# Performance work log

Hardware: AMD Instinct MI355X
Metric: run time of the kernel (lower is better)

The kernel has to match this reference:

```python
import jax, jax.numpy as jnp
import numpy as np
from jax import lax

B, P, E, H, V, S = 128, 196, 2048, 512, 10000, 21


def setup_inputs() -> dict:
    key = jax.random.key(0)
    ks = jax.random.split(key, 16)
    r = lambda k, shape, s=0.02: (jax.random.normal(k, shape, jnp.float32) * s)
    return {
        "img_features": jax.random.normal(ks[0], (B, P, E), jnp.float32),
        "captions": jax.random.randint(ks[1], (B, S), 0, V),
        "U_w": r(ks[2], (H, H)), "U_b": jnp.zeros((H,), jnp.float32),
        "W_w": r(ks[3], (E, H)), "W_b": jnp.zeros((H,), jnp.float32),
        "v_w": r(ks[4], (H, 1)), "v_b": jnp.zeros((1,), jnp.float32),
        "init_h_w": r(ks[5], (E, H)), "init_h_b": jnp.zeros((H,), jnp.float32),
        "init_c_w": r(ks[6], (E, H)), "init_c_b": jnp.zeros((H,), jnp.float32),
        "f_beta_w": r(ks[7], (H, E)), "f_beta_b": jnp.zeros((E,), jnp.float32),
        "out_w": r(ks[8], (H, V)), "out_b": jnp.zeros((V,), jnp.float32),
        "emb": r(ks[9], (V, H)),
        "lstm_Wih": r(ks[10], (H + E, 4 * H)), "lstm_Whh": r(ks[11], (H, 4 * H)),
        "lstm_bih": jnp.zeros((4 * H,), jnp.float32), "lstm_bhh": jnp.zeros((4 * H,), jnp.float32),
    }


def reference(img_features, captions, U_w, U_b, W_w, W_b, v_w, v_b,
              init_h_w, init_h_b, init_c_w, init_c_b, f_beta_w, f_beta_b,
              out_w, out_b, emb, lstm_Wih, lstm_Whh, lstm_bih, lstm_bhh):
    batch = img_features.shape[0]
    T = captions.shape[1] - 1  # max_timespan (static)

    # init LSTM state from mean-pooled image features
    avg = img_features.mean(axis=1)                       # [B, E]
    h0 = jnp.tanh(avg @ init_h_w + init_h_b)              # [B, H]
    c0 = jnp.tanh(avg @ init_c_w + init_c_b)              # [B, H]

    # precompute W(img_features) once; it does not depend on h
    W_s = img_features @ W_w + W_b                        # [B, P, H]

    # in training mode the original feeds the embedding of word 0 every step
    emb0 = jnp.broadcast_to(emb[0], (batch, emb.shape[1]))  # [B, H]

    def step(carry, _):
        h, c = carry
        # additive attention
        att = jnp.tanh(W_s + (h @ U_w + U_b)[:, None, :])      # [B, P, H]
        e = (att @ v_w)[..., 0] + v_b[0]                        # [B, P]
        alpha = jax.nn.softmax(e, axis=1)                       # [B, P]
        context = jnp.einsum('bp,bpe->be', alpha, img_features) # [B, E]
        # gated context
        gate = jax.nn.sigmoid(h @ f_beta_w + f_beta_b)          # [B, E]
        x = jnp.concatenate([emb0, gate * context], axis=1)     # [B, H+E]
        # LSTMCell (torch gate order i, f, g, o)
        gates = x @ lstm_Wih + lstm_bih + h @ lstm_Whh + lstm_bhh  # [B, 4H]
        i, f, g, o = jnp.split(gates, 4, axis=1)
        i = jax.nn.sigmoid(i); f = jax.nn.sigmoid(f)
        g = jnp.tanh(g); o = jax.nn.sigmoid(o)
        c_new = f * c + i * g
        h_new = o * jnp.tanh(c_new)
        out = h_new @ out_w + out_b                             # [B, V] (dropout = identity, eval)
        return (h_new, c_new), (out, alpha)

    (_, _), (preds, alphas) = lax.scan(step, (h0, c0), None, length=T)
    preds = jnp.transpose(preds, (1, 0, 2))    # [B, T, V]
    alphas = jnp.transpose(alphas, (1, 0, 2))  # [B, T, P]
    return preds, alphas
```

## Files before the change

### kernel.cpp

```cpp
#include <hip/hip_runtime.h>
#include <stdint.h>


typedef unsigned short u16;
typedef unsigned int u32;
typedef __attribute__((ext_vector_type(8))) short bf16x8;
typedef __attribute__((ext_vector_type(4))) float f32x4;

__device__ __forceinline__ float bf2f(u16 u) { return __uint_as_float(((u32)u) << 16); }
__device__ __forceinline__ u16 f2bf(float f) {
  u32 x = __float_as_uint(f);
  u32 r = x + 0x7fffu + ((x >> 16) & 1u);
  return (u16)(r >> 16);
}
__device__ __forceinline__ float tanh_f(float x) {
  x = fminf(15.f, fmaxf(-15.f, x));
  float e = __expf(2.f * x);
  return 1.f - 2.f * __builtin_amdgcn_rcpf(e + 1.f);
}
__device__ __forceinline__ float sigm_f(float x) {
  x = fminf(30.f, fmaxf(-30.f, x));
  return __builtin_amdgcn_rcpf(1.f + __expf(-x));
}

__global__ __launch_bounds__(256) void k_f32_to_bf16(const float* __restrict__ in,
                                                     u16* __restrict__ out) {
  size_t i = ((size_t)blockIdx.x * 256 + threadIdx.x) * 8;
  float4 v0 = *(const float4*)(in + i);
  float4 v1 = *(const float4*)(in + i + 4);
  union { u16 u[8]; uint4 v; } r;
  r.u[0] = f2bf(v0.x); r.u[1] = f2bf(v0.y); r.u[2] = f2bf(v0.z); r.u[3] = f2bf(v0.w);
  r.u[4] = f2bf(v1.x); r.u[5] = f2bf(v1.y); r.u[6] = f2bf(v1.z); r.u[7] = f2bf(v1.w);
  *(uint4*)(out + i) = r.v;
}

__global__ __launch_bounds__(256) void k_avg(const u16* __restrict__ imgb,
                                             u16* __restrict__ avgb) {
  int b = blockIdx.y;
  int c0 = blockIdx.x * 512 + threadIdx.x * 2;
  const u32* p0 = (const u32*)(imgb + (size_t)b * 196 * 2048 + c0);
  float s0 = 0.f, s1 = 0.f;
  for (int p = 0; p < 196; ++p) {
    u32 v = p0[(size_t)p * 1024];
    s0 += bf2f((u16)(v & 0xffff));
    s1 += bf2f((u16)(v >> 16));
  }
  const float inv = 1.f / 196.f;
  u32 o = ((u32)f2bf(s1 * inv) << 16) | (u32)f2bf(s0 * inv);
  *(u32*)(avgb + (size_t)b * 2048 + c0) = o;
}

__global__ __launch_bounds__(256) void k_transpose_bf16(const float* __restrict__ in,
                                                        int R, int C, int Cpad,
                                                        u16* __restrict__ out, int out_ld) {
  __shared__ float tile[32][33];
  int c0 = blockIdx.x * 32, r0 = blockIdx.y * 32;
  int tx = threadIdx.x, ty = threadIdx.y;
#pragma unroll
  for (int i = 0; i < 32; i += 8) {
    int r = r0 + ty + i, c = c0 + tx;
    tile[ty + i][tx] = (r < R && c < C) ? in[(size_t)r * C + c] : 0.f;
  }
  __syncthreads();
#pragma unroll
  for (int i = 0; i < 32; i += 8) {
    int c = c0 + ty + i, r = r0 + tx;
    if (c < Cpad && r < R) out[(size_t)c * out_ld + r] = f2bf(tile[tx][ty + i]);
  }
}

__global__ __launch_bounds__(256) void k_cbias(const float* __restrict__ emb,
                                               const float* __restrict__ Wih,
                                               const float* __restrict__ bih,
                                               const float* __restrict__ bhh,
                                               float* __restrict__ cb) {
  __shared__ float e0[512];
  int tid = threadIdx.x;
  for (int i = tid; i < 512; i += 256) e0[i] = emb[i];
  __syncthreads();
  int n = blockIdx.x * 256 + tid;
  float s = bih[n] + bhh[n];
  for (int k = 0; k < 512; ++k) s += e0[k] * Wih[(size_t)k * 2048 + n];
  cb[n] = s;
}

enum { EPI_WS = 0, EPI_TANH_H, EPI_TANH_C, EPI_F32, EPI_GATE, EPI_OUT };

template <int EPI>
__global__ __launch_bounds__(256) void k_gemm64(
    const u16* __restrict__ A, const u16* __restrict__ BT, int K, int Ntiles,
    const float* __restrict__ bias, float* __restrict__ outF, u16* __restrict__ outB,
    u16* __restrict__ outB2, const float* __restrict__ ctx, long out_ld, int ncap) {
  __shared__ __align__(16) u16 Asm[64 * 72];
  __shared__ __align__(16) u16 Bsm[64 * 72];
  int bid = blockIdx.x;
  int mt = bid / Ntiles, nt = bid % Ntiles;
  long m0 = (long)mt * 64, n0 = (long)nt * 64;
  int tid = threadIdx.x, lane = tid & 63, w = tid >> 6;
  int srow = tid >> 3, schk = tid & 7;
  f32x4 acc[4] = {};
  const u16* Ap0 = A + (m0 + srow) * K + schk * 8;
  const u16* Ap1 = A + (m0 + srow + 32) * K + schk * 8;
  const u16* Bp0 = BT + (n0 + srow) * K + schk * 8;
  const u16* Bp1 = BT + (n0 + srow + 32) * K + schk * 8;
  u16* Aw0 = Asm + srow * 72 + schk * 8;
  u16* Aw1 = Asm + (srow + 32) * 72 + schk * 8;
  u16* Bw0 = Bsm + srow * 72 + schk * 8;
  u16* Bw1 = Bsm + (srow + 32) * 72 + schk * 8;
  const u16* Ar = Asm + (w * 16 + (lane & 15)) * 72 + (lane >> 4) * 8;
  const u16* Br = Bsm + (lane & 15) * 72 + (lane >> 4) * 8;
  for (int k0 = 0; k0 < K; k0 += 64) {
    uint4 a0 = *(const uint4*)(Ap0 + k0);
    uint4 a1 = *(const uint4*)(Ap1 + k0);
    uint4 b0 = *(const uint4*)(Bp0 + k0);
    uint4 b1 = *(const uint4*)(Bp1 + k0);
    __syncthreads();
    *(uint4*)Aw0 = a0;
    *(uint4*)Aw1 = a1;
    *(uint4*)Bw0 = b0;
    *(uint4*)Bw1 = b1;
    __syncthreads();
#pragma unroll
    for (int kk = 0; kk < 2; ++kk) {
      bf16x8 af = *(const bf16x8*)(Ar + kk * 32);
#pragma unroll
      for (int sn = 0; sn < 4; ++sn) {
        bf16x8 bfr = *(const bf16x8*)(Br + sn * 16 * 72 + kk * 32);
        acc[sn] = __builtin_amdgcn_mfma_f32_16x16x32_bf16(af, bfr, acc[sn], 0, 0, 0);
      }
    }
  }
  int cb = lane & 15, rb = (lane >> 4) * 4;
#pragma unroll
  for (int sn = 0; sn < 4; ++sn) {
#pragma unroll
    for (int r = 0; r < 4; ++r) {
      long m = m0 + w * 16 + rb + r;
      long n = n0 + sn * 16 + cb;
      float v = acc[sn][r];
      if (EPI == EPI_WS) {
        outB[m * 512 + n] = f2bf(v + bias[n]);
      } else if (EPI == EPI_TANH_H) {
        u16 hv = f2bf(tanh_f(v + bias[n]));
        outB[m * 512 + n] = hv;
        outB2[m * 2560 + n] = hv;
      } else if (EPI == EPI_TANH_C) {
        outF[m * 512 + n] = tanh_f(v + bias[n]);
      } else if (EPI == EPI_F32) {
        outF[m * out_ld + n] = v + bias[n];
      } else if (EPI == EPI_GATE) {
        float g = sigm_f(v + bias[n]);
        outB[m * 2560 + n] = f2bf(g * ctx[m * 2048 + n]);
      } else {
        if (n < ncap) outF[m * out_ld + n] = v + bias[n];
      }
    }
  }
}

__global__ __launch_bounds__(512) void k_attn_e(const u16* __restrict__ Ws,
                                                const float* __restrict__ hU,
                                                const float* __restrict__ v_w,
                                                float* __restrict__ alpha_buf,
                                                float* __restrict__ alphas_out) {
  int b = blockIdx.x, tid = threadIdx.x, lane = tid & 63, w = tid >> 6;
  __shared__ float hU_s[512], v_s[512], e_s[200];
  hU_s[tid] = hU[b * 512 + tid];
  v_s[tid] = v_w[tid];
  __syncthreads();
  for (int p = w; p < 196; p += 8) {
    uint4 pk = *(const uint4*)(Ws + ((size_t)b * 196 + p) * 512 + lane * 8);
    const u16* u = (const u16*)&pk;
    float s = 0.f;
#pragma unroll
    for (int j = 0; j < 8; ++j) {
      int h = lane * 8 + j;
      s += tanh_f(bf2f(u[j]) + hU_s[h]) * v_s[h];
    }
#pragma unroll
    for (int off = 32; off; off >>= 1) s += __shfl_xor(s, off);
    if (lane == 0) e_s[p] = s;
  }
  __syncthreads();
  if (w == 0) {
    float mx = -1e30f;
    for (int q = lane; q < 196; q += 64) mx = fmaxf(mx, e_s[q]);
#pragma unroll
    for (int off = 32; off; off >>= 1) mx = fmaxf(mx, __shfl_xor(mx, off));
    float ssum = 0.f;
    for (int q = lane; q < 196; q += 64) {
      float ex = __expf(e_s[q] - mx);
      e_s[q] = ex;
      ssum += ex;
    }
#pragma unroll
    for (int off = 32; off; off >>= 1) ssum += __shfl_xor(ssum, off);
    float inv = 1.f / ssum;
    for (int q = lane; q < 196; q += 64) e_s[q] *= inv;
  }
  __syncthreads();
  if (tid < 196) {
    float a = e_s[tid];
    alpha_buf[b * 196 + tid] = a;
    alphas_out[(size_t)b * 3920 + tid] = a;
  }
}

__global__ __launch_bounds__(512) void k_context(const float* __restrict__ alpha_buf,
                                                 const u16* __restrict__ imgb,
                                                 float* __restrict__ ctx) {
  int b = blockIdx.x >> 1, half = blockIdx.x & 1, tid = threadIdx.x;
  __shared__ float al[196];
  if (tid < 196) al[tid] = alpha_buf[b * 196 + tid];
  __syncthreads();
  int c0 = half * 1024 + tid * 2;
  const u32* base = (const u32*)(imgb + (size_t)b * 196 * 2048 + c0);
  float a0 = 0.f, a1 = 0.f;
#pragma unroll 4
  for (int p = 0; p < 196; ++p) {
    u32 v = base[(size_t)p * 1024];
    float ap = al[p];
    a0 += ap * bf2f((u16)(v & 0xffff));
    a1 += ap * bf2f((u16)(v >> 16));
  }
  ctx[(size_t)b * 2048 + c0] = a0;
  ctx[(size_t)b * 2048 + c0 + 1] = a1;
}

__global__ __launch_bounds__(256) void k_lstm_cell(const float* __restrict__ gates,
                                                   float* __restrict__ c,
                                                   u16* __restrict__ hb,
                                                   u16* __restrict__ Abuf) {
  int idx = blockIdx.x * 256 + threadIdx.x;
  int b = idx >> 9, n = idx & 511;
  const float* g = gates + (size_t)b * 2048;
  float i = sigm_f(g[n]);
  float f = sigm_f(g[512 + n]);
  float gg = tanh_f(g[1024 + n]);
  float o = sigm_f(g[1536 + n]);
  float cn = f * c[idx] + i * gg;
  float h = o * tanh_f(cn);
  c[idx] = cn;
  u16 hv = f2bf(h);
  hb[idx] = hv;
  Abuf[(size_t)b * 2560 + 2048 + n] = hv;
}

extern "C" void kernel_launch(void* const* d_in, const int* in_sizes, int n_in,
                              void* d_out, int out_size, void* d_ws, size_t ws_size,
                              hipStream_t stream) {
  const float* img = (const float*)d_in[0];
  const float* U_w = (const float*)d_in[2];
  const float* U_b = (const float*)d_in[3];
  const float* W_w = (const float*)d_in[4];
  const float* W_b = (const float*)d_in[5];
  const float* v_w = (const float*)d_in[6];
  const float* ih_w = (const float*)d_in[8];
  const float* ih_b = (const float*)d_in[9];
  const float* ic_w = (const float*)d_in[10];
  const float* ic_b = (const float*)d_in[11];
  const float* fb_w = (const float*)d_in[12];
  const float* fb_b = (const float*)d_in[13];
  const float* out_w = (const float*)d_in[14];
  const float* out_b = (const float*)d_in[15];
  const float* emb = (const float*)d_in[16];
  const float* Wih = (const float*)d_in[17];
  const float* Whh = (const float*)d_in[18];
  const float* bih = (const float*)d_in[19];
  const float* bhh = (const float*)d_in[20];
  float* preds = (float*)d_out;
  float* alphas = (float*)d_out + 25600000;

  char* ws = (char*)d_ws;
  size_t off = 0;
  auto alloc = [&](size_t bytes) {
    void* p = ws + off;
    off = (off + bytes + 255) & ~(size_t)255;
    return p;
  };
  u16* imgb = (u16*)alloc((size_t)128 * 196 * 2048 * 2);
  u16* avgb = (u16*)alloc((size_t)128 * 2048 * 2);
  u16* WsB = (u16*)alloc((size_t)128 * 196 * 512 * 2);
  u16* WwT = (u16*)alloc((size_t)512 * 2048 * 2);
  u16* UwT = (u16*)alloc((size_t)512 * 512 * 2);
  u16* ihT = (u16*)alloc((size_t)512 * 2048 * 2);
  u16* icT = (u16*)alloc((size_t)512 * 2048 * 2);
  u16* fbT = (u16*)alloc((size_t)2048 * 512 * 2);
  u16* WcT = (u16*)alloc((size_t)2048 * 2560 * 2);
  u16* owT = (u16*)alloc((size_t)10048 * 512 * 2);
  float* cbias = (float*)alloc(2048 * 4);
  u16* hb = (u16*)alloc((size_t)128 * 512 * 2);
  float* cbuf = (float*)alloc((size_t)128 * 512 * 4);
  float* hU = (float*)alloc((size_t)128 * 512 * 4);
  float* albuf = (float*)alloc((size_t)128 * 196 * 4);
  float* ctx = (float*)alloc((size_t)128 * 2048 * 4);
  u16* Abuf = (u16*)alloc((size_t)128 * 2560 * 2);
  float* gates = (float*)alloc((size_t)128 * 2048 * 4);
  if (off > ws_size) return;
  (void)in_sizes; (void)n_in; (void)out_size;

  dim3 tb(32, 8);
  k_f32_to_bf16<<<25088, 256, 0, stream>>>(img, imgb);
  k_avg<<<dim3(4, 128), 256, 0, stream>>>(imgb, avgb);
  k_transpose_bf16<<<dim3(16, 64), tb, 0, stream>>>(W_w, 2048, 512, 512, WwT, 2048);
  k_transpose_bf16<<<dim3(16, 16), tb, 0, stream>>>(U_w, 512, 512, 512, UwT, 512);
  k_transpose_bf16<<<dim3(16, 64), tb, 0, stream>>>(ih_w, 2048, 512, 512, ihT, 2048);
  k_transpose_bf16<<<dim3(16, 64), tb, 0, stream>>>(ic_w, 2048, 512, 512, icT, 2048);
  k_transpose_bf16<<<dim3(64, 16), tb, 0, stream>>>(fb_w, 512, 2048, 2048, fbT, 512);
  k_transpose_bf16<<<dim3(314, 16), tb, 0, stream>>>(out_w, 512, 10000, 10048, owT, 512);
  k_transpose_bf16<<<dim3(64, 64), tb, 0, stream>>>(Wih + 512 * 2048, 2048, 2048, 2048, WcT, 2560);
  k_transpose_bf16<<<dim3(64, 16), tb, 0, stream>>>(Whh, 512, 2048, 2048, WcT + 2048, 2560);
  k_cbias<<<8, 256, 0, stream>>>(emb, Wih, bih, bhh, cbias);
  k_gemm64<EPI_WS><<<392 * 8, 256, 0, stream>>>(imgb, WwT, 2048, 8, W_b, nullptr, WsB,
                                                nullptr, nullptr, 0L, 0);
  k_gemm64<EPI_TANH_H><<<16, 256, 0, stream>>>(avgb, ihT, 2048, 8, ih_b, nullptr, hb,
                                               Abuf + 2048, nullptr, 0L, 0);
  k_gemm64<EPI_TANH_C><<<16, 256, 0, stream>>>(avgb, icT, 2048, 8, ic_b, cbuf, nullptr,
                                               nullptr, nullptr, 0L, 0);

  for (int t = 0; t < 20; ++t) {
    k_gemm64<EPI_F32><<<16, 256, 0, stream>>>(hb, UwT, 512, 8, U_b, hU, nullptr,
                                              nullptr, nullptr, 512L, 0);
    k_attn_e<<<128, 512, 0, stream>>>(WsB, hU, v_w, albuf, alphas + (size_t)t * 196);
    k_context<<<256, 512, 0, stream>>>(albuf, imgb, ctx);
    k_gemm64<EPI_GATE><<<64, 256, 0, stream>>>(hb, fbT, 512, 32, fb_b, nullptr, Abuf,
                                               nullptr, ctx, 0L, 0);
    k_gemm64<EPI_F32><<<64, 256, 0, stream>>>(Abuf, WcT, 2560, 32, cbias, gates,
                                              nullptr, nullptr, nullptr, 2048L, 0);
    k_lstm_cell<<<256, 256, 0, stream>>>(gates, cbuf, hb, Abuf);
    k_gemm64<EPI_OUT><<<2 * 157, 256, 0, stream>>>(hb, owT, 512, 157, out_b,
                                                   preds + (size_t)t * 10000, nullptr,
                                                   nullptr, nullptr, 200000L, 10000);
  }
}
```

Baseline: 2.584 ms.

## Fuse attention and context, fold LSTM cell into gate GEMM, batch output projection

Merges the h·U projection, attention scores, softmax and context reduction into one per-batch kernel. The LSTM cell moves into the gate GEMM epilogue, which relies on permuting the combined weight columns and bias so each tile holds interleaved i/f/g/o. All hidden states are saved so the vocabulary projection runs once after the loop as a single 128x128-tile GEMM, and the W_s GEMM also uses that larger tile. Double-buffered A inputs avoid a race between steps. This cuts per-step launches from seven to three and replaces twenty small output GEMMs with one large one, at the cost of a serial 512x512 matvec inside each attention block.

```diff
diff --git a/kernel.cpp b/kernel.cpp
--- a/kernel.cpp
+++ b/kernel.cpp
@@ -50,6 +50,7 @@
   *(u32*)(avgb + (size_t)b * 2048 + c0) = o;
 }
 
+template <bool PERM>
 __global__ __launch_bounds__(256) void k_transpose_bf16(const float* __restrict__ in,
                                                         int R, int C, int Cpad,
                                                         u16* __restrict__ out, int out_ld) {
@@ -65,7 +66,10 @@
 #pragma unroll
   for (int i = 0; i < 32; i += 8) {
     int c = c0 + ty + i, r = r0 + tx;
-    if (c < Cpad && r < R) out[(size_t)c * out_ld + r] = f2bf(tile[tx][ty + i]);
+    if (c < Cpad && r < R) {
+      int co = PERM ? ((c & 511) * 4 + (c >> 9)) : c;
+      out[(size_t)co * out_ld + r] = f2bf(tile[tx][ty + i]);
+    }
   }
 }
 
@@ -81,16 +85,17 @@
   int n = blockIdx.x * 256 + tid;
   float s = bih[n] + bhh[n];
   for (int k = 0; k < 512; ++k) s += e0[k] * Wih[(size_t)k * 2048 + n];
-  cb[n] = s;
-}
-
-enum { EPI_WS = 0, EPI_TANH_H, EPI_TANH_C, EPI_F32, EPI_GATE, EPI_OUT };
+  cb[(n & 511) * 4 + (n >> 9)] = s;
+}
+
+enum { EPI_TANH_H = 0, EPI_TANH_C, EPI_GATE, EPI_LSTM };
 
 template <int EPI>
 __global__ __launch_bounds__(256) void k_gemm64(
     const u16* __restrict__ A, const u16* __restrict__ BT, int K, int Ntiles,
-    const float* __restrict__ bias, float* __restrict__ outF, u16* __restrict__ outB,
-    u16* __restrict__ outB2, const float* __restrict__ ctx, long out_ld, int ncap) {
+    const float* __restrict__ bias, float* __restrict__ outF,
+    u16* __restrict__ outB, u16* __restrict__ outB2, u16* __restrict__ outB3,
+    const float* __restrict__ ctx, int tstep) {
   __shared__ __align__(16) u16 Asm[64 * 72];
   __shared__ __align__(16) u16 Bsm[64 * 72];
   int bid = blockIdx.x;
@@ -131,119 +136,202 @@
     }
   }
   int cb = lane & 15, rb = (lane >> 4) * 4;
-#pragma unroll
-  for (int sn = 0; sn < 4; ++sn) {
-#pragma unroll
-    for (int r = 0; r < 4; ++r) {
-      long m = m0 + w * 16 + rb + r;
-      long n = n0 + sn * 16 + cb;
-      float v = acc[sn][r];
-      if (EPI == EPI_WS) {
-        outB[m * 512 + n] = f2bf(v + bias[n]);
-      } else if (EPI == EPI_TANH_H) {
-        u16 hv = f2bf(tanh_f(v + bias[n]));
-        outB[m * 512 + n] = hv;
-        outB2[m * 2560 + n] = hv;
-      } else if (EPI == EPI_TANH_C) {
-        outF[m * 512 + n] = tanh_f(v + bias[n]);
-      } else if (EPI == EPI_F32) {
-        outF[m * out_ld + n] = v + bias[n];
-      } else if (EPI == EPI_GATE) {
-        float g = sigm_f(v + bias[n]);
-        outB[m * 2560 + n] = f2bf(g * ctx[m * 2048 + n]);
-      } else {
-        if (n < ncap) outF[m * out_ld + n] = v + bias[n];
+  if constexpr (EPI == EPI_LSTM) {
+    __shared__ float gtile[64][68];
+#pragma unroll
+    for (int sn = 0; sn < 4; ++sn)
+#pragma unroll
+      for (int r = 0; r < 4; ++r)
+        gtile[w * 16 + rb + r][sn * 16 + cb] = acc[sn][r] + bias[n0 + sn * 16 + cb];
+    __syncthreads();
+#pragma unroll
+    for (int i = 0; i < 4; ++i) {
+      int idx = tid * 4 + i;
+      int m = idx >> 4, chl = idx & 15;
+      float iv = gtile[m][chl * 4 + 0];
+      float fv = gtile[m][chl * 4 + 1];
+      float gv = gtile[m][chl * 4 + 2];
+      float ov = gtile[m][chl * 4 + 3];
+      long bg = m0 + m;
+      int ch = (int)(n0 >> 2) + chl;
+      long ci = bg * 512 + ch;
+      float cn = sigm_f(fv) * outF[ci] + sigm_f(iv) * tanh_f(gv);
+      float h = sigm_f(ov) * tanh_f(cn);
+      outF[ci] = cn;
+      u16 hv = f2bf(h);
+      outB[ci] = hv;
+      outB2[bg * 2560 + 2048 + ch] = hv;
+      outB3[((long)tstep * 128 + bg) * 512 + ch] = hv;
+    }
+  } else {
+#pragma unroll
+    for (int sn = 0; sn < 4; ++sn) {
+#pragma unroll
+      for (int r = 0; r < 4; ++r) {
+        long m = m0 + w * 16 + rb + r;
+        long n = n0 + sn * 16 + cb;
+        float v = acc[sn][r];
+        if (EPI == EPI_TANH_H) {
+          u16 hv = f2bf(tanh_f(v + bias[n]));
+          outB[m * 512 + n] = hv;
+          outB2[m * 2560 + 2048 + n] = hv;
+        } else if (EPI == EPI_TANH_C) {
+          outF[m * 512 + n] = tanh_f(v + bias[n]);
+        } else {
+          outB[m * 2560 + n] = f2bf(sigm_f(v + bias[n]) * ctx[m * 2048 + n]);
+        }
       }
     }
   }
 }
 
-__global__ __launch_bounds__(512) void k_attn_e(const u16* __restrict__ Ws,
-                                                const float* __restrict__ hU,
-                                                const float* __restrict__ v_w,
-                                                float* __restrict__ alpha_buf,
-                                                float* __restrict__ alphas_out) {
+enum { EPI128_WS = 0, EPI128_OUT };
+
+template <int EPI>
+__global__ __launch_bounds__(256) void k_gemm128(
+    const u16* __restrict__ A, const u16* __restrict__ BT, int K, int Ntiles,
+    const float* __restrict__ bias, float* __restrict__ outF,
+    u16* __restrict__ outB, int ncap) {
+  __shared__ __align__(16) u16 Asm[128 * 72];
+  __shared__ __align__(16) u16 Bsm[128 * 72];
+  int bid = blockIdx.x;
+  int mt = bid / Ntiles, nt = bid % Ntiles;
+  long m0 = (long)mt * 128, n0 = (long)nt * 128;
+  int tid = threadIdx.x, lane = tid & 63, w = tid >> 6;
+  int wr = w >> 1, wc = w & 1;
+  int srow = tid >> 3, schk = tid & 7;
+  f32x4 acc[4][4] = {};
+  const u16* Ap = A + (m0 + srow) * K + schk * 8;
+  const u16* Bp = BT + (n0 + srow) * K + schk * 8;
+  u16* Aw = Asm + srow * 72 + schk * 8;
+  u16* Bw = Bsm + srow * 72 + schk * 8;
+  const u16* Ar = Asm + (wr * 64 + (lane & 15)) * 72 + (lane >> 4) * 8;
+  const u16* Br = Bsm + (wc * 64 + (lane & 15)) * 72 + (lane >> 4) * 8;
+  for (int k0 = 0; k0 < K; k0 += 64) {
+    uint4 a0 = *(const uint4*)(Ap + k0);
+    uint4 a1 = *(const uint4*)(Ap + (size_t)32 * K + k0);
+    uint4 a2 = *(const uint4*)(Ap + (size_t)64 * K + k0);
+    uint4 a3 = *(const uint4*)(Ap + (size_t)96 * K + k0);
+    uint4 b0 = *(const uint4*)(Bp + k0);
+    uint4 b1 = *(const uint4*)(Bp + (size_t)32 * K + k0);
+    uint4 b2 = *(const uint4*)(Bp + (size_t)64 * K + k0);
+    uint4 b3 = *(const uint4*)(Bp + (size_t)96 * K + k0);
+    __syncthreads();
+    *(uint4*)Aw = a0;
+    *(uint4*)(Aw + 32 * 72) = a1;
+    *(uint4*)(Aw + 64 * 72) = a2;
+    *(uint4*)(Aw + 96 * 72) = a3;
+    *(uint4*)Bw = b0;
+    *(uint4*)(Bw + 32 * 72) = b1;
+    *(uint4*)(Bw + 64 * 72) = b2;
+    *(uint4*)(Bw + 96 * 72) = b3;
+    __syncthreads();
+#pragma unroll
+    for (int kk = 0; kk < 2; ++kk) {
+      bf16x8 af[4], bfv[4];
+#pragma unroll
+      for (int i = 0; i < 4; ++i) {
+        af[i] = *(const bf16x8*)(Ar + i * 16 * 72 + kk * 32);
+        bfv[i] = *(const bf16x8*)(Br + i * 16 * 72 + kk * 32);
+      }
+#pragma unroll
+      for (int sm = 0; sm < 4; ++sm)
+#pragma unroll
+        for (int sn = 0; sn < 4; ++sn)
+          acc[sm][sn] = __builtin_amdgcn_mfma_f32_16x16x32_bf16(af[sm], bfv[sn],
+                                                                acc[sm][sn], 0, 0, 0);
+    }
+  }
+  int cb = lane & 15, rb = (lane >> 4) * 4;
+#pragma unroll
+  for (int sm = 0; sm < 4; ++sm) {
+#pragma unroll
+    for (int sn = 0; sn < 4; ++sn) {
+#pragma unroll
+      for (int r = 0; r < 4; ++r) {
+        long m = m0 + wr * 64 + sm * 16 + rb + r;
+        long n = n0 + wc * 64 + sn * 16 + cb;
+        float v = acc[sm][sn][r];
+        if (EPI == EPI128_WS) {
+          outB[m * 512 + n] = f2bf(v + bias[n]);
+        } else {
+          if (n < ncap) {
+            long t = m >> 7, b = m & 127;
+            outF[b * 200000 + t * 10000 + n] = v + bias[n];
+          }
+        }
+      }
+    }
+  }
+}
+
+__global__ __launch_bounds__(512) void k_attn_ctx(
+    const u16* __restrict__ hb, const u16* __restrict__ UwB,
+    const float* __restrict__ U_b, const float* __restrict__ v_w,
+    const u16* __restrict__ WsB, const u16* __restrict__ imgb,
+    float* __restrict__ ctx, float* __restrict__ alphas_t) {
   int b = blockIdx.x, tid = threadIdx.x, lane = tid & 63, w = tid >> 6;
-  __shared__ float hU_s[512], v_s[512], e_s[200];
-  hU_s[tid] = hU[b * 512 + tid];
+  __shared__ float h_s[512], hu_s[512], v_s[512], al_s[200];
+  h_s[tid] = bf2f(hb[b * 512 + tid]);
   v_s[tid] = v_w[tid];
   __syncthreads();
+  {
+    float s = U_b[tid];
+    const u16* up = UwB + tid;
+#pragma unroll 8
+    for (int k = 0; k < 512; ++k) s += h_s[k] * bf2f(up[(size_t)k * 512]);
+    hu_s[tid] = s;
+  }
+  __syncthreads();
   for (int p = w; p < 196; p += 8) {
-    uint4 pk = *(const uint4*)(Ws + ((size_t)b * 196 + p) * 512 + lane * 8);
+    uint4 pk = *(const uint4*)(WsB + ((size_t)b * 196 + p) * 512 + lane * 8);
     const u16* u = (const u16*)&pk;
-    float s = 0.f;
+    float e = 0.f;
 #pragma unroll
     for (int j = 0; j < 8; ++j) {
-      int h = lane * 8 + j;
-      s += tanh_f(bf2f(u[j]) + hU_s[h]) * v_s[h];
-    }
-#pragma unroll
-    for (int off = 32; off; off >>= 1) s += __shfl_xor(s, off);
-    if (lane == 0) e_s[p] = s;
+      int hch = lane * 8 + j;
+      e += tanh_f(bf2f(u[j]) + hu_s[hch]) * v_s[hch];
+    }
+#pragma unroll
+    for (int off = 32; off; off >>= 1) e += __shfl_xor(e, off);
+    if (lane == 0) al_s[p] = e;
   }
   __syncthreads();
   if (w == 0) {
     float mx = -1e30f;
-    for (int q = lane; q < 196; q += 64) mx = fmaxf(mx, e_s[q]);
+    for (int q = lane; q < 196; q += 64) mx = fmaxf(mx, al_s[q]);
 #pragma unroll
     for (int off = 32; off; off >>= 1) mx = fmaxf(mx, __shfl_xor(mx, off));
     float ssum = 0.f;
     for (int q = lane; q < 196; q += 64) {
-      float ex = __expf(e_s[q] - mx);
-      e_s[q] = ex;
+      float ex = __expf(al_s[q] - mx);
+      al_s[q] = ex;
       ssum += ex;
     }
 #pragma unroll
     for (int off = 32; off; off >>= 1) ssum += __shfl_xor(ssum, off);
     float inv = 1.f / ssum;
-    for (int q = lane; q < 196; q += 64) e_s[q] *= inv;
-  }
-  __syncthreads();
-  if (tid < 196) {
-    float a = e_s[tid];
-    alpha_buf[b * 196 + tid] = a;
-    alphas_out[(size_t)b * 3920 + tid] = a;
-  }
-}
-
-__global__ __launch_bounds__(512) void k_context(const float* __restrict__ alpha_buf,
-                                                 const u16* __restrict__ imgb,
-                                                 float* __restrict__ ctx) {
-  int b = blockIdx.x >> 1, half = blockIdx.x & 1, tid = threadIdx.x;
-  __shared__ float al[196];
-  if (tid < 196) al[tid] = alpha_buf[b * 196 + tid];
-  __syncthreads();
-  int c0 = half * 1024 + tid * 2;
-  const u32* base = (const u32*)(imgb + (size_t)b * 196 * 2048 + c0);
-  float a0 = 0.f, a1 = 0.f;
-#pragma unroll 4
+    for (int q = lane; q < 196; q += 64) al_s[q] *= inv;
+  }
+  __syncthreads();
+  if (tid < 196) alphas_t[(size_t)b * 3920 + tid] = al_s[tid];
+  const u32* ib = (const u32*)(imgb + (size_t)b * 196 * 2048) + tid;
+  float a0 = 0.f, a1 = 0.f, a2 = 0.f, a3 = 0.f;
+#pragma unroll 2
   for (int p = 0; p < 196; ++p) {
-    u32 v = base[(size_t)p * 1024];
-    float ap = al[p];
-    a0 += ap * bf2f((u16)(v & 0xffff));
-    a1 += ap * bf2f((u16)(v >> 16));
-  }
-  ctx[(size_t)b * 2048 + c0] = a0;
-  ctx[(size_t)b * 2048 + c0 + 1] = a1;
-}
-
-__global__ __launch_bounds__(256) void k_lstm_cell(const float* __restrict__ gates,
-                                                   float* __restrict__ c,
-                                                   u16* __restrict__ hb,
-                                                   u16* __restrict__ Abuf) {
-  int idx = blockIdx.x * 256 + threadIdx.x;
-  int b = idx >> 9, n = idx & 511;
-  const float* g = gates + (size_t)b * 2048;
-  float i = sigm_f(g[n]);
-  float f = sigm_f(g[512 + n]);
-  float gg = tanh_f(g[1024 + n]);
-  float o = sigm_f(g[1536 + n]);
-  float cn = f * c[idx] + i * gg;
-  float h = o * tanh_f(cn);
-  c[idx] = cn;
-  u16 hv = f2bf(h);
-  hb[idx] = hv;
-  Abuf[(size_t)b * 2560 + 2048 + n] = hv;
+    float ap = al_s[p];
+    u32 v0 = ib[(size_t)p * 1024];
+    u32 v1 = ib[(size_t)p * 1024 + 512];
+    a0 += ap * bf2f((u16)(v0 & 0xffff));
+    a1 += ap * bf2f((u16)(v0 >> 16));
+    a2 += ap * bf2f((u16)(v1 & 0xffff));
+    a3 += ap * bf2f((u16)(v1 >> 16));
+  }
+  float* cp = ctx + (size_t)b * 2048;
+  cp[tid * 2] = a0;
+  cp[tid * 2 + 1] = a1;
+  cp[1024 + tid * 2] = a2;
+  cp[1024 + tid * 2 + 1] = a3;
 }
 
 extern "C" void kernel_launch(void* const* d_in, const int* in_sizes, int n_in,
@@ -282,54 +370,50 @@
   u16* avgb = (u16*)alloc((size_t)128 * 2048 * 2);
   u16* WsB = (u16*)alloc((size_t)128 * 196 * 512 * 2);
   u16* WwT = (u16*)alloc((size_t)512 * 2048 * 2);
-  u16* UwT = (u16*)alloc((size_t)512 * 512 * 2);
+  u16* UwB = (u16*)alloc((size_t)512 * 512 * 2);
   u16* ihT = (u16*)alloc((size_t)512 * 2048 * 2);
   u16* icT = (u16*)alloc((size_t)512 * 2048 * 2);
   u16* fbT = (u16*)alloc((size_t)2048 * 512 * 2);
   u16* WcT = (u16*)alloc((size_t)2048 * 2560 * 2);
-  u16* owT = (u16*)alloc((size_t)10048 * 512 * 2);
+  u16* owT = (u16*)alloc((size_t)10112 * 512 * 2);
   float* cbias = (float*)alloc(2048 * 4);
   u16* hb = (u16*)alloc((size_t)128 * 512 * 2);
   float* cbuf = (float*)alloc((size_t)128 * 512 * 4);
-  float* hU = (float*)alloc((size_t)128 * 512 * 4);
-  float* albuf = (float*)alloc((size_t)128 * 196 * 4);
   float* ctx = (float*)alloc((size_t)128 * 2048 * 4);
-  u16* Abuf = (u16*)alloc((size_t)128 * 2560 * 2);
-  float* gates = (float*)alloc((size_t)128 * 2048 * 4);
+  u16* AbufA = (u16*)alloc((size_t)128 * 2560 * 2);
+  u16* AbufB = (u16*)alloc((size_t)128 * 2560 * 2);
+  u16* hAll = (u16*)alloc((size_t)2560 * 512 * 2);
   if (off > ws_size) return;
   (void)in_sizes; (void)n_in; (void)out_size;
 
   dim3 tb(32, 8);
   k_f32_to_bf16<<<25088, 256, 0, stream>>>(img, imgb);
+  k_f32_to_bf16<<<128, 256, 0, stream>>>(U_w, UwB);
   k_avg<<<dim3(4, 128), 256, 0, stream>>>(imgb, avgb);
-  k_transpose_bf16<<<dim3(16, 64), tb, 0, stream>>>(W_w, 2048, 512, 512, WwT, 2048);
-  k_transpose_bf16<<<dim3(16, 16), tb, 0, stream>>>(U_w, 512, 512, 512, UwT, 512);
-  k_transpose_bf16<<<dim3(16, 64), tb, 0, stream>>>(ih_w, 2048, 512, 512, ihT, 2048);
-  k_transpose_bf16<<<dim3(16, 64), tb, 0, stream>>>(ic_w, 2048, 512, 512, icT, 2048);
-  k_transpose_bf16<<<dim3(64, 16), tb, 0, stream>>>(fb_w, 512, 2048, 2048, fbT, 512);
-  k_transpose_bf16<<<dim3(314, 16), tb, 0, stream>>>(out_w, 512, 10000, 10048, owT, 512);
-  k_transpose_bf16<<<dim3(64, 64), tb, 0, stream>>>(Wih + 512 * 2048, 2048, 2048, 2048, WcT, 2560);
-  k_transpose_bf16<<<dim3(64, 16), tb, 0, stream>>>(Whh, 512, 2048, 2048, WcT + 2048, 2560);
+  k_transpose_bf16<false><<<dim3(16, 64), tb, 0, stream>>>(W_w, 2048, 512, 512, WwT, 2048);
+  k_transpose_bf16<false><<<dim3(16, 64), tb, 0, stream>>>(ih_w, 2048, 512, 512, ihT, 2048);
+  k_transpose_bf16<false><<<dim3(16, 64), tb, 0, stream>>>(ic_w, 2048, 512, 512, icT, 2048);
+  k_transpose_bf16<false><<<dim3(64, 16), tb, 0, stream>>>(fb_w, 512, 2048, 2048, fbT, 512);
+  k_transpose_bf16<false><<<dim3(316, 16), tb, 0, stream>>>(out_w, 512, 10000, 10112, owT, 512);
+  k_transpose_bf16<true><<<dim3(64, 64), tb, 0, stream>>>(Wih + 512 * 2048, 2048, 2048, 2048, WcT, 2560);
+  k_transpose_bf16<true><<<dim3(64, 16), tb, 0, stream>>>(Whh, 512, 2048, 2048, WcT + 2048, 2560);
   k_cbias<<<8, 256, 0, stream>>>(emb, Wih, bih, bhh, cbias);
-  k_gemm64<EPI_WS><<<392 * 8, 256, 0, stream>>>(imgb, WwT, 2048, 8, W_b, nullptr, WsB,
-                                                nullptr, nullptr, 0L, 0);
+  k_gemm128<EPI128_WS><<<784, 256, 0, stream>>>(imgb, WwT, 2048, 4, W_b, nullptr, WsB, 0);
   k_gemm64<EPI_TANH_H><<<16, 256, 0, stream>>>(avgb, ihT, 2048, 8, ih_b, nullptr, hb,
-                                               Abuf + 2048, nullptr, 0L, 0);
+                                               AbufA, nullptr, nullptr, 0);
   k_gemm64<EPI_TANH_C><<<16, 256, 0, stream>>>(avgb, icT, 2048, 8, ic_b, cbuf, nullptr,
-                                               nullptr, nullptr, 0L, 0);
+                                               nullptr, nullptr, nullptr, 0);
 
   for (int t = 0; t < 20; ++t) {
-    k_gemm64<EPI_F32><<<16, 256, 0, stream>>>(hb, UwT, 512, 8, U_b, hU, nullptr,
-                                              nullptr, nullptr, 512L, 0);
-    k_attn_e<<<128, 512, 0, stream>>>(WsB, hU, v_w, albuf, alphas + (size_t)t * 196);
-    k_context<<<256, 512, 0, stream>>>(albuf, imgb, ctx);
-    k_gemm64<EPI_GATE><<<64, 256, 0, stream>>>(hb, fbT, 512, 32, fb_b, nullptr, Abuf,
-                                               nullptr, ctx, 0L, 0);
-    k_gemm64<EPI_F32><<<64, 256, 0, stream>>>(Abuf, WcT, 2560, 32, cbias, gates,
-                                              nullptr, nullptr, nullptr, 2048L, 0);
-    k_lstm_cell<<<256, 256, 0, stream>>>(gates, cbuf, hb, Abuf);
-    k_gemm64<EPI_OUT><<<2 * 157, 256, 0, stream>>>(hb, owT, 512, 157, out_b,
-                                                   preds + (size_t)t * 10000, nullptr,
-                                                   nullptr, nullptr, 200000L, 10000);
-  }
-}
+    u16* Acur = (t & 1) ? AbufB : AbufA;
+    u16* Anxt = (t & 1) ? AbufA : AbufB;
+    k_attn_ctx<<<128, 512, 0, stream>>>(hb, UwB, U_b, v_w, WsB, imgb, ctx,
+                                        alphas + (size_t)t * 196);
+    k_gemm64<EPI_GATE><<<64, 256, 0, stream>>>(hb, fbT, 512, 32, fb_b, nullptr, Acur,
+                                               nullptr, nullptr, ctx, 0);
+    k_gemm64<EPI_LSTM><<<64, 256, 0, stream>>>(Acur, WcT, 2560, 32, cbias, cbuf, hb,
+                                               Anxt, hAll, nullptr, t);
+  }
+  k_gemm128<EPI128_OUT><<<20 * 79, 256, 0, stream>>>(hAll, owT, 512, 79, out_b,
+                                                     preds, nullptr, 10000);
+}
```

Result: slower. 2.833 ms (+9.6%).
